# Kernel tuning notes

Hardware: AMD Instinct MI355X
Metric: run time of the kernel (lower is better)

## Reference

```python
import jax, jax.numpy as jnp
import numpy as np

D_MODEL = 1024
N_HEAD = 16
HEAD_SIZE = D_MODEL // N_HEAD
LAYER_ID = 12
N_LAYER = 24
HEAD_SIZE_DIVISOR = 8
TM_DIM = 32   # TIME_MIX_EXTRA_DIM
TD_DIM = 64   # TIME_DECAY_EXTRA_DIM
B, T = 4, 1024
EPS = 1e-5 * HEAD_SIZE_DIVISOR ** 2


def setup_inputs() -> dict:
    key = jax.random.key(0)
    ks = jax.random.split(key, 12)
    C = D_MODEL
    r0 = LAYER_ID / (N_LAYER - 1)
    r1 = 1.0 - LAYER_ID / N_LAYER
    ddd = np.arange(C, dtype=np.float64) / C
    time_maa_x = (1.0 - ddd ** r1).astype(np.float32)
    time_maa_w = (1.0 - ddd ** r1).astype(np.float32)
    time_maa_k = (1.0 - ddd ** r1).astype(np.float32)
    time_maa_v = (1.0 - (ddd ** r1 + 0.3 * r0)).astype(np.float32)
    time_maa_r = (1.0 - ddd ** (0.5 * r1)).astype(np.float32)
    time_maa_g = (1.0 - ddd ** (0.5 * r1)).astype(np.float32)
    n = np.arange(C, dtype=np.float64)
    time_decay = (-6.0 + 5.0 * (n / (C - 1)) ** (0.7 + 1.3 * r0)).astype(np.float32)
    zig = ((n + 1) % 3 - 1) * 0.1
    time_faaaa = (r0 * (1 - n / (C - 1)) + zig).astype(np.float32).reshape(N_HEAD, HEAD_SIZE)
    s = 1.0 / np.sqrt(C)
    inp = {
        "x": jax.random.normal(ks[0], (B, T, C), jnp.float32),
        "time_maa_x": jnp.asarray(time_maa_x),
        "time_maa_w": jnp.asarray(time_maa_w),
        "time_maa_k": jnp.asarray(time_maa_k),
        "time_maa_v": jnp.asarray(time_maa_v),
        "time_maa_r": jnp.asarray(time_maa_r),
        "time_maa_g": jnp.asarray(time_maa_g),
        "time_maa_w1": jax.random.uniform(ks[1], (C, TM_DIM * 5), jnp.float32, -0.01, 0.01),
        "time_maa_w2": jax.random.uniform(ks[2], (5, TM_DIM, C), jnp.float32, -0.01, 0.01),
        "time_decay": jnp.asarray(time_decay),
        "time_decay_w1": jax.random.uniform(ks[3], (C, TD_DIM), jnp.float32, -0.01, 0.01),
        "time_decay_w2": jax.random.uniform(ks[4], (TD_DIM, C), jnp.float32, -0.01, 0.01),
        "time_faaaa": jnp.asarray(time_faaaa),
        "W_r": jax.random.normal(ks[5], (C, C), jnp.float32) * s,
        "W_k": jax.random.normal(ks[6], (C, C), jnp.float32) * s,
        "W_v": jax.random.normal(ks[7], (C, C), jnp.float32) * s,
        "W_g": jax.random.normal(ks[8], (C, C), jnp.float32) * s,
        "W_o": jax.random.normal(ks[9], (C, C), jnp.float32) * s,
        "ln_gamma": jnp.ones((C,), jnp.float32),
        "ln_beta": jnp.zeros((C,), jnp.float32),
    }
    return inp


def _wkv6(r, k, v, w, u):
    # r,k,v,w: (B,T,H,K); u: (H,K). Sequential data-dependent linear attention.
    Bc, Tc, H, K = r.shape
    wdec = jnp.exp(-jnp.exp(w))  # decay in (0,1)

    def step(S, inp):
        r_t, k_t, v_t, wd_t = inp           # each (B,H,K)
        kv = k_t[:, :, :, None] * v_t[:, :, None, :]   # (B,H,K,K) key x value
        y = jnp.einsum('bhk,bhkj->bhj', r_t, S + u[None, :, :, None] * kv)
        S = S * wd_t[:, :, :, None] + kv    # decay along key dim, then accumulate
        return S, y

    S0 = jnp.zeros((Bc, H, K, K), r.dtype)
    xs = (jnp.swapaxes(r, 0, 1), jnp.swapaxes(k, 0, 1),
          jnp.swapaxes(v, 0, 1), jnp.swapaxes(wdec, 0, 1))
    _, ys = jax.lax.scan(step, S0, xs)      # ys: (T,B,H,K)
    return jnp.swapaxes(ys, 0, 1).reshape(Bc, Tc, H * K)


def reference(x, time_maa_x, time_maa_w, time_maa_k, time_maa_v, time_maa_r,
              time_maa_g, time_maa_w1, time_maa_w2, time_decay, time_decay_w1,
              time_decay_w2, time_faaaa, W_r, W_k, W_v, W_g, W_o, ln_gamma, ln_beta):
    Bc, Tc, C = x.shape
    H, K = N_HEAD, HEAD_SIZE
    # token shift: state[t] = x[t-1], zero at t=0
    xs = jnp.pad(x, ((0, 0), (1, 0), (0, 0)))[:, :-1]
    xx = xs - x
    # LoRA-style data-dependent mixing coefficients
    xxx = x + xx * time_maa_x
    m = jnp.tanh(xxx @ time_maa_w1).reshape(Bc, Tc, 5, TM_DIM)
    m = jnp.einsum('btfe,fec->fbtc', m, time_maa_w2)  # (5,B,T,C)
    mw, mk, mv, mr, mg = m[0], m[1], m[2], m[3], m[4]
    xw = x + xx * (time_maa_w + mw)
    xk = x + xx * (time_maa_k + mk)
    xv = x + xx * (time_maa_v + mv)
    xr = x + xx * (time_maa_r + mr)
    xg = x + xx * (time_maa_g + mg)
    r = xr @ W_r
    k = xk @ W_k
    v = xv @ W_v
    g = jax.nn.silu(xg @ W_g)
    w = time_decay + jnp.tanh(xw @ time_decay_w1) @ time_decay_w2
    y = _wkv6(r.reshape(Bc, Tc, H, K), k.reshape(Bc, Tc, H, K),
              v.reshape(Bc, Tc, H, K), w.reshape(Bc, Tc, H, K), time_faaaa)
    # GroupNorm with H groups over channel dim (per (b,t) position)
    yg = y.reshape(Bc, Tc, H, K)
    mu = jnp.mean(yg, axis=-1, keepdims=True)
    var = jnp.mean((yg - mu) ** 2, axis=-1, keepdims=True)
    yn = ((yg - mu) / jnp.sqrt(var + EPS)).reshape(Bc, Tc, C)
    yn = yn * ln_gamma + ln_beta
    return (yn * g) @ W_o
```

## Files before the change

kernel.cpp:

```cpp
#include <hip/hip_runtime.h>

#define Bb 4
#define Tt 1024
#define Cc 1024
#define Hh 16
#define BT (Bb*Tt)
#define CHUNK 32
#define NCH (Tt/CHUNK)

typedef unsigned int uint;
typedef unsigned short u16;
typedef __bf16 bf16x8 __attribute__((ext_vector_type(8)));
typedef float f32x4 __attribute__((ext_vector_type(4)));
typedef const __attribute__((address_space(1))) uint GU;
typedef __attribute__((address_space(3))) uint LU;

__device__ __forceinline__ float blo(uint u) { return __uint_as_float(u << 16); }
__device__ __forceinline__ float bhi(uint u) { return __uint_as_float(u & 0xffff0000u); }
__device__ __forceinline__ float b2f(u16 u) { return __uint_as_float(((uint)u) << 16); }
__device__ __forceinline__ u16 f2b(float f) {
  uint u = __float_as_uint(f);
  return (u16)((u + 0x7fffu + ((u >> 16) & 1u)) >> 16);
}
__device__ __forceinline__ float fast_tanh(float x) {
  float e = __expf(2.f * x);
  return 1.f - 2.f / (e + 1.f);
}

struct WPair { const float* s; u16* d; int K; int N; };
struct WPack { WPair p[9]; };

__global__ __launch_bounds__(256) void prep_transW(WPack wp,
    const float* __restrict__ x, const float* __restrict__ maa_x,
    u16* __restrict__ xxx)
{
  __shared__ float tile[32][33];
  if (blockIdx.z < 9) {
    WPair pr = wp.p[blockIdx.z];
    int c0 = blockIdx.x*32, r0 = blockIdx.y*32;
    if (c0 >= pr.N || r0 >= pr.K) return;
    int tc = threadIdx.x & 31, tr = threadIdx.x >> 5;
    #pragma unroll
    for (int p = 0; p < 4; ++p)
      tile[tr + p*8][tc] = pr.s[(size_t)(r0 + tr + p*8)*pr.N + c0 + tc];
    __syncthreads();
    #pragma unroll
    for (int p = 0; p < 4; ++p) {
      int n = tr + p*8;
      pr.d[(size_t)(c0 + n)*pr.K + r0 + tc] = f2b(tile[tc][n]);
    }
  } else {
    int vb = (blockIdx.z - 9)*1024 + blockIdx.y*32 + blockIdx.x;
    int idx = vb*256 + threadIdx.x;
    int c4 = idx & 255;
    int bt = idx >> 8;
    int t = bt & (Tt-1);
    float4 xc = ((const float4*)x)[idx];
    float4 xp = make_float4(0.f,0.f,0.f,0.f);
    if (t > 0) xp = ((const float4*)x)[idx - 256];
    float4 mx = ((const float4*)maa_x)[c4];
    ushort4 o;
    o.x = f2b(fmaf(xp.x - xc.x, mx.x, xc.x));
    o.y = f2b(fmaf(xp.y - xc.y, mx.y, xc.y));
    o.z = f2b(fmaf(xp.z - xc.z, mx.z, xc.z));
    o.w = f2b(fmaf(xp.w - xc.w, mx.w, xc.w));
    ((ushort4*)xxx)[idx] = o;
  }
}

__global__ __launch_bounds__(256) void mix_mfma(
    const float* __restrict__ x, const float* __restrict__ m1p,
    const u16* __restrict__ w2T,
    const float* __restrict__ maa_w, const float* __restrict__ maa_k,
    const float* __restrict__ maa_v, const float* __restrict__ maa_r,
    const float* __restrict__ maa_g,
    u16* __restrict__ xw, u16* __restrict__ xk, u16* __restrict__ xv,
    u16* __restrict__ xr, u16* __restrict__ xg)
{
  __shared__ __align__(16) u16 strip[4][16][72];
  const int tid = threadIdx.x;
  const int lane = tid & 63;
  const int wv = tid >> 6;
  const int sid = blockIdx.x*4 + wv;
  const int rs = sid >> 4, cs = sid & 15;
  const int r0 = rs*16, c0 = cs*64;
  const int fr = lane & 15, kc = lane >> 4;

  float xc[4][4], xd[4][4];
  #pragma unroll
  for (int n = 0; n < 4; ++n) {
    int col = c0 + n*16 + fr;
    #pragma unroll
    for (int q = 0; q < 4; ++q) {
      int row = r0 + kc*4 + q;
      size_t o = (size_t)row*Cc + col;
      float v = x[o];
      float p = ((row & (Tt-1)) != 0) ? x[o - Cc] : 0.f;
      xc[n][q] = v;
      xd[n][q] = p - v;
    }
  }

  const size_t aBase = (size_t)(r0 + fr)*160 + kc*8;
  u16* const outs[5] = {xw, xk, xv, xr, xg};
  const float* const maas[5] = {maa_w, maa_k, maa_v, maa_r, maa_g};

  #pragma unroll
  for (int f = 0; f < 5; ++f) {
    float s8[8] = {0.f,0.f,0.f,0.f,0.f,0.f,0.f,0.f};
    #pragma unroll
    for (int z = 0; z < 4; ++z) {
      const float4* p = (const float4*)(m1p + (size_t)z*655360 + aBase + f*32);
      float4 a = p[0], b = p[1];
      s8[0]+=a.x; s8[1]+=a.y; s8[2]+=a.z; s8[3]+=a.w;
      s8[4]+=b.x; s8[5]+=b.y; s8[6]+=b.z; s8[7]+=b.w;
    }
    u16 t8[8];
    #pragma unroll
    for (int j = 0; j < 8; ++j) t8[j] = f2b(fast_tanh(s8[j]));
    bf16x8 af = *(const bf16x8*)t8;
    f32x4 acc[4];
    #pragma unroll
    for (int n = 0; n < 4; ++n) {
      bf16x8 bg = *(const bf16x8*)(w2T + (size_t)(c0 + n*16 + fr)*160 + f*32 + kc*8);
      acc[n] = __builtin_amdgcn_mfma_f32_16x16x32_bf16(af, bg, f32x4{0.f,0.f,0.f,0.f}, 0, 0, 0);
    }
    const float* __restrict__ ma = maas[f];
    u16* __restrict__ op = outs[f];
    #pragma unroll
    for (int n = 0; n < 4; ++n) {
      int colL = n*16 + fr;
      float mv = ma[c0 + colL];
      #pragma unroll
      for (int q = 0; q < 4; ++q)
        strip[wv][kc*4 + q][colL] = f2b(fmaf(xd[n][q], mv + acc[n][q], xc[n][q]));
    }
    #pragma unroll
    for (int rd = 0; rd < 2; ++rd) {
      int r8 = (lane >> 3) + rd*8;
      uint4 v = *(const uint4*)&strip[wv][r8][(lane & 7)*8];
      *(uint4*)(op + (size_t)(r0 + r8)*Cc + c0 + (lane & 7)*8) = v;
    }
  }
}

template<bool OUTF32>
__device__ __forceinline__ void mfma_core(
    const u16* __restrict__ A, const u16* __restrict__ Bt,
    void* __restrict__ Cout, const float* __restrict__ bias,
    int ld, int kloop, int N, int act)
{
  __shared__ __align__(16) u16 lds[2][2][128*32];
  const int tid = threadIdx.x;
  const int lane = tid & 63;
  const int wv = __builtin_amdgcn_readfirstlane(tid >> 6);

  const int nby8 = gridDim.y >> 3;
  const int i_lin = blockIdx.y * gridDim.x + blockIdx.x;
  const int cx = i_lin & 7, rest = i_lin >> 3;
  const int bm = (cx * nby8 + rest % nby8) * 128;
  const int bn = (rest / nby8) * 128;

  const int wm = (wv >> 1) * 64;
  const int wn = (wv & 1) * 64;
  const int kc = lane >> 4;
  const int fr = lane & 15;

  const int srow = wv*16 + (lane >> 2);
  const int ssw  = (srow >> 1) & 3;
  const int scol = ((lane & 3) ^ ssw) * 8;
  const size_t aoff = (size_t)(bm + srow) * ld + scol;
  const size_t boff = (size_t)(bn + srow) * ld + scol;

#define STAGE(bufi, kt) do { \
    size_t ko_ = (size_t)(kt) * 32; \
    __builtin_amdgcn_global_load_lds((GU*)(A + aoff + ko_), \
        (LU*)&lds[bufi][0][wv*512], 16, 0, 0); \
    __builtin_amdgcn_global_load_lds((GU*)(A + aoff + (size_t)64*ld + ko_), \
        (LU*)&lds[bufi][0][wv*512 + 64*32], 16, 0, 0); \
    __builtin_amdgcn_global_load_lds((GU*)(Bt + boff + ko_), \
        (LU*)&lds[bufi][1][wv*512], 16, 0, 0); \
    __builtin_amdgcn_global_load_lds((GU*)(Bt + boff + (size_t)64*ld + ko_), \
        (LU*)&lds[bufi][1][wv*512 + 64*32], 16, 0, 0); \
  } while(0)

  int ard[4], brd[4];
  #pragma unroll
  for (int m = 0; m < 4; ++m) {
    int ra = wm + m*16 + fr;
    int rb = wn + m*16 + fr;
    ard[m] = ra*32 + (kc ^ ((ra >> 1) & 3))*8;
    brd[m] = rb*32 + (kc ^ ((rb >> 1) & 3))*8;
  }

  f32x4 acc[4][4];
  #pragma unroll
  for (int m = 0; m < 4; ++m)
    #pragma unroll
    for (int n = 0; n < 4; ++n)
      acc[m][n] = f32x4{0.f, 0.f, 0.f, 0.f};

  const int NK = kloop >> 5;
  STAGE(0, 0);
  __syncthreads();
  int buf = 0;
  for (int kt = 0; kt < NK; ++kt) {
    if (kt + 1 < NK) STAGE(buf^1, kt+1);
    bf16x8 af[4], bg[4];
    #pragma unroll
    for (int m = 0; m < 4; ++m) af[m] = *(const bf16x8*)&lds[buf][0][ard[m]];
    #pragma unroll
    for (int n = 0; n < 4; ++n) bg[n] = *(const bf16x8*)&lds[buf][1][brd[n]];
    #pragma unroll
    for (int m = 0; m < 4; ++m)
      #pragma unroll
      for (int n = 0; n < 4; ++n)
        acc[m][n] = __builtin_amdgcn_mfma_f32_16x16x32_bf16(af[m], bg[n], acc[m][n], 0, 0, 0);
    __syncthreads();
    buf ^= 1;
  }
#undef STAGE

  const int orow = bm + wm + (lane >> 4) * 4;
  const int ocol = bn + wn + fr;
  #pragma unroll
  for (int m = 0; m < 4; ++m) {
    #pragma unroll
    for (int n = 0; n < 4; ++n) {
      int col = ocol + n*16;
      if (col < N) {
        float bs = bias ? bias[col] : 0.f;
        #pragma unroll
        for (int q = 0; q < 4; ++q) {
          float vv = acc[m][n][q] + bs;
          if (act == 1) vv = tanhf(vv);
          else if (act == 2) vv = vv / (1.f + __expf(-vv));
          size_t off = (size_t)(orow + m*16 + q) * N + col;
          if (OUTF32) ((float*)Cout)[off] = vv;
          else ((u16*)Cout)[off] = f2b(vv);
        }
      }
    }
  }
}

template<int ACT, bool OUTF32>
__global__ __launch_bounds__(256) void gemm_mfma(
    const u16* __restrict__ A, const u16* __restrict__ Bt,
    void* __restrict__ Cout, const float* __restrict__ bias, int K, int N)
{
  mfma_core<OUTF32>(A, Bt, Cout, bias, K, K, N, ACT);
}

__global__ __launch_bounds__(256) void gemm_ksplit(
    const u16* __restrict__ A, const u16* __restrict__ Bt,
    float* __restrict__ Cp, int ld, int ksz, int N)
{
  const int z = blockIdx.z;
  mfma_core<true>(A + (size_t)z*ksz, Bt + (size_t)z*ksz,
                  Cp + (size_t)z*4096*N, nullptr, ld, ksz, N, 0);
}

struct GPack { const u16* A[4]; const u16* B[4]; u16* C[4]; };

#define VMW(n) asm volatile("s_waitcnt vmcnt(" #n ")" ::: "memory")
#define LGKM0() asm volatile("s_waitcnt lgkmcnt(0)" ::: "memory")
#define SCHB() __builtin_amdgcn_sched_barrier(0)
#define HBAR() __builtin_amdgcn_s_barrier()

__global__ __launch_bounds__(512) void gemm_rkvg256(GPack gp) {
  __shared__ __align__(16) u16 lds[2][2][2][8192];
  const int z = blockIdx.z;
  const u16* __restrict__ Ap  = gp.A[z];
  const u16* __restrict__ Btp = gp.B[z];
  u16* __restrict__ Cp = gp.C[z];
  const int act = (z == 3) ? 2 : 0;

  const int tid = threadIdx.x;
  const int lane = tid & 63;
  const int wv = __builtin_amdgcn_readfirstlane(tid >> 6);

  const int i_lin = blockIdx.y * gridDim.x + blockIdx.x;
  const int tile = (i_lin & 7) * 8 + (i_lin >> 3);
  const int bm = (tile >> 2) * 256;
  const int bn = (tile & 3) * 256;

  const int wm = (wv >> 2) * 128;
  const int wn = (wv & 3) * 64;
  const int kc = lane >> 4;
  const int fr = lane & 15;

  const int srow0 = (wv*2 + 0)*16 + (lane >> 2);
  const int srow1 = (wv*2 + 1)*16 + (lane >> 2);
  const int sc0 = ((lane & 3) ^ ((srow0 >> 1) & 3)) * 8;
  const int sc1 = ((lane & 3) ^ ((srow1 >> 1) & 3)) * 8;
  const size_t aoff0 = (size_t)(bm + srow0)*Cc + sc0;
  const size_t aoff1 = (size_t)(bm + srow1)*Cc + sc1;
  const size_t boff0 = (size_t)(bn + srow0)*Cc + sc0;
  const size_t boff1 = (size_t)(bn + srow1)*Cc + sc1;

  int ard[8], brd[4];
  #pragma unroll
  for (int mh = 0; mh < 2; ++mh)
    #pragma unroll
    for (int mf = 0; mf < 4; ++mf) {
      int r = wm + mh*64 + mf*16 + fr;
      ard[mh*4+mf] = r*32 + (kc ^ ((r >> 1) & 3))*8;
    }
  #pragma unroll
  for (int nf = 0; nf < 4; ++nf) {
    int r = wn + nf*16 + fr;
    brd[nf] = r*32 + (kc ^ ((r >> 1) & 3))*8;
  }

  f32x4 acc[8][4];
  #pragma unroll
  for (int m = 0; m < 8; ++m)
    #pragma unroll
    for (int n = 0; n < 4; ++n)
      acc[m][n] = f32x4{0.f, 0.f, 0.f, 0.f};

#define STG256(DB, MAT, KH, kt, off0, off1, src) do { \
    u16* dst_ = &lds[(DB)][(MAT)][(KH)][wv*1024]; \
    __builtin_amdgcn_global_load_lds((GU*)((src) + (off0) + (size_t)(kt)*64 + (KH)*32), \
        (LU*)dst_, 16, 0, 0); \
    __builtin_amdgcn_global_load_lds((GU*)((src) + (off1) + (size_t)(kt)*64 + (KH)*32), \
        (LU*)(dst_ + 512), 16, 0, 0); \
  } while(0)

#define PH256(cur, KH, MH, LOADB, STMAT, STKH, DOSTAGE, VMTOK) do { \
    _Pragma("unroll") \
    for (int mf = 0; mf < 4; ++mf) \
      af[mf] = *(const bf16x8*)&lds[(cur)][0][KH][ard[(MH)*4+mf]]; \
    if (LOADB) { \
      _Pragma("unroll") \
      for (int nf = 0; nf < 4; ++nf) \
        bg[nf] = *(const bf16x8*)&lds[(cur)][1][KH][brd[nf]]; \
    } \
    if (DOSTAGE) { \
      if ((STMAT) == 0) STG256((cur)^1, 0, STKH, t+1, aoff0, aoff1, Ap); \
      else              STG256((cur)^1, 1, STKH, t+1, boff0, boff1, Btp); \
    } \
    VMTOK; \
    SCHB(); \
    HBAR(); \
    LGKM0(); \
    SCHB(); \
    __builtin_amdgcn_s_setprio(1); \
    _Pragma("unroll") \
    for (int mf = 0; mf < 4; ++mf) \
      _Pragma("unroll") \
      for (int nf = 0; nf < 4; ++nf) \
        acc[(MH)*4+mf][nf] = __builtin_amdgcn_mfma_f32_16x16x32_bf16(af[mf], bg[nf], acc[(MH)*4+mf][nf], 0, 0, 0); \
    __builtin_amdgcn_s_setprio(0); \
    SCHB(); \
    HBAR(); \
  } while(0)

  const int NK = Cc >> 6;

  STG256(0, 0, 0, 0, aoff0, aoff1, Ap);
  STG256(0, 1, 0, 0, boff0, boff1, Btp);
  STG256(0, 0, 1, 0, aoff0, aoff1, Ap);
  STG256(0, 1, 1, 0, boff0, boff1, Btp);
  VMW(4);
  SCHB();
  HBAR();

  bf16x8 af[4], bg[4];
  int t;
  #pragma unroll 2
  for (t = 0; t < NK - 1; ++t) {
    const int cur = t & 1;
    PH256(cur, 0, 0, true,  0, 0, true,  (void)0);
    PH256(cur, 0, 1, false, 1, 0, true,  VMW(4));
    PH256(cur, 1, 0, true,  0, 1, true,  (void)0);
    PH256(cur, 1, 1, false, 1, 1, true,  VMW(4));
  }
  {
    const int cur = t & 1;
    PH256(cur, 0, 0, true,  0, 0, false, (void)0);
    PH256(cur, 0, 1, false, 0, 0, false, VMW(0));
    PH256(cur, 1, 0, true,  0, 0, false, (void)0);
    PH256(cur, 1, 1, false, 0, 0, false, (void)0);
  }
#undef PH256
#undef STG256

  const int orow = bm + wm + (lane >> 4) * 4;
  const int ocol = bn + wn + fr;
  #pragma unroll
  for (int m = 0; m < 8; ++m) {
    #pragma unroll
    for (int nf = 0; nf < 4; ++nf) {
      #pragma unroll
      for (int q = 0; q < 4; ++q) {
        float vv = acc[m][nf][q];
        if (act == 2) vv = vv / (1.f + __expf(-vv));
        Cp[(size_t)(orow + (m >> 2)*64 + (m & 3)*16 + q) * Cc + ocol + nf*16] = f2b(vv);
      }
    }
  }
}

__global__ __launch_bounds__(256) void wkv_pass1(u16* __restrict__ r,
    const u16* __restrict__ k, const u16* __restrict__ v,
    const float* __restrict__ wl1p, const u16* __restrict__ tdw2T,
    const float* __restrict__ tdecay, const float* __restrict__ u,
    u16* __restrict__ y, u16* __restrict__ S, float* __restrict__ D)
{
  __shared__ __align__(16) u16 rS[CHUNK][72];
  __shared__ __align__(16) u16 kS[CHUNK][72];
  __shared__ __align__(16) u16 vS[CHUNK][72];
  __shared__ __align__(16) u16 aW[CHUNK][72];
  __shared__ __align__(16) float bufEW[CHUNK][68];
  __shared__ __align__(16) float eKnL[CHUNK][68];
  __shared__ __align__(16) u16 Rt[CHUNK][72];
  __shared__ __align__(16) u16 Kt[CHUNK][72];
  __shared__ __align__(16) u16 Ru[CHUNK][72];
  __shared__ __align__(16) u16 KhT[64][40];
  __shared__ __align__(16) u16 VT[64][40];
  __shared__ __align__(16) u16 A_lds[CHUNK][40];
  __shared__ float uL[64];
  __shared__ float Dl[64];

  const int blk = blockIdx.x;
  const int chunk = blk & (NCH-1);
  const int bh = blk >> 5;
  const int h = bh & (Hh-1);
  const int b = bh >> 4;
  const int tid = threadIdx.x;
  const int lane = tid & 63;
  const int wv = tid >> 6;
  const int fr = lane & 15;
  const int kc = lane >> 4;

  const int trow0 = b*Tt + chunk*CHUNK;
  const size_t rowbase = (size_t)trow0*Cc + h*64;
  {
    int tt = tid >> 3, c8 = (tid & 7)*8;
    size_t go = rowbase + (size_t)tt*Cc + c8;
    *(uint4*)&rS[tt][c8] = *(const uint4*)(r + go);
    *(uint4*)&kS[tt][c8] = *(const uint4*)(k + go);
    *(uint4*)&vS[tt][c8] = *(const uint4*)(v + go);
    size_t wrow = (size_t)(trow0 + tt)*64 + c8;
    float s8[8] = {0.f,0.f,0.f,0.f,0.f,0.f,0.f,0.f};
    #pragma unroll
    for (int z = 0; z < 4; ++z) {
      const float4* p = (const float4*)(wl1p + (size_t)z*262144 + wrow);
      float4 a = p[0], b2 = p[1];
      s8[0]+=a.x; s8[1]+=a.y; s8[2]+=a.z; s8[3]+=a.w;
      s8[4]+=b2.x; s8[5]+=b2.y; s8[6]+=b2.z; s8[7]+=b2.w;
    }
    u16 t8[8];
    #pragma unroll
    for (int j = 0; j < 8; ++j) t8[j] = f2b(fast_tanh(s8[j]));
    *(uint4*)&aW[tt][c8] = *(const uint4*)t8;
  }
  if (tid < 64) uL[tid] = u[h*64 + tid];
  __syncthreads();

  {
    const int icol = wv*16 + fr;
    const float bs = tdecay[h*64 + icol];
    #pragma unroll
    for (int tb = 0; tb < 2; ++tb) {
      f32x4 acc = {0.f,0.f,0.f,0.f};
      #pragma unroll
      for (int ks = 0; ks < 2; ++ks) {
        bf16x8 a  = *(const bf16x8*)&aW[tb*16+fr][kc*8 + ks*32];
        bf16x8 bb = *(const bf16x8*)(tdw2T + (size_t)(h*64 + icol)*64 + ks*32 + kc*8);
        acc = __builtin_amdgcn_mfma_f32_16x16x32_bf16(a, bb, acc, 0, 0, 0);
      }
      #pragma unroll
      for (int q = 0; q < 4; ++q)
        bufEW[tb*16 + kc*4 + q][icol] = __expf(acc[q] + bs);
    }
  }
  __syncthreads();

  if (tid < 64) {
    float eR = 1.f;
    for (int t = 0; t < CHUNK; ++t) {
      float e = bufEW[t][tid];
      bufEW[t][tid] = eR;
      eR *= __expf(-e);
      eKnL[t][tid] = __builtin_amdgcn_rcpf(eR);
    }
    Dl[tid] = eR;
    D[(size_t)blk*64 + tid] = eR;
  }
  __syncthreads();

  {
    int t = tid >> 3, i0 = (tid & 7)*8;
    uint4 rv4 = *(const uint4*)&rS[t][i0];
    uint4 kv4 = *(const uint4*)&kS[t][i0];
    const uint* rw = (const uint*)&rv4;
    const uint* kw = (const uint*)&kv4;
    u16 rt8[8], kt8[8], ru8[8];
    #pragma unroll
    for (int q = 0; q < 8; ++q) {
      int i = i0 + q;
      float rv = (q & 1) ? bhi(rw[q>>1]) : blo(rw[q>>1]);
      float kv = (q & 1) ? bhi(kw[q>>1]) : blo(kw[q>>1]);
      float eR = bufEW[t][i];
      float eKn = eKnL[t][i];
      float ktv = kv * eKn;
      rt8[q] = f2b(rv * eR);
      kt8[q] = f2b(ktv);
      ru8[q] = f2b(rv * uL[i]);
      KhT[i][t] = f2b(ktv * Dl[i]);
      VT[i][t] = vS[t][i];
    }
    *(uint4*)&Rt[t][i0] = *(const uint4*)rt8;
    *(uint4*)&Kt[t][i0] = *(const uint4*)kt8;
    *(uint4*)&Ru[t][i0] = *(const uint4*)ru8;
  }
  __syncthreads();

  {
    const int wr = wv >> 1, wc = wv & 1;
    f32x4 accA = {0.f,0.f,0.f,0.f};
    f32x4 accD = {0.f,0.f,0.f,0.f};
    #pragma unroll
    for (int ks = 0; ks < 2; ++ks) {
      bf16x8 a  = *(const bf16x8*)&Rt[wr*16+fr][kc*8 + ks*32];
      bf16x8 bb = *(const bf16x8*)&Kt[wc*16+fr][kc*8 + ks*32];
      accA = __builtin_amdgcn_mfma_f32_16x16x32_bf16(a, bb, accA, 0, 0, 0);
      bf16x8 a2 = *(const bf16x8*)&Ru[wr*16+fr][kc*8 + ks*32];
      bf16x8 b2 = *(const bf16x8*)&kS[wc*16+fr][kc*8 + ks*32];
      accD = __builtin_amdgcn_mfma_f32_16x16x32_bf16(a2, b2, accD, 0, 0, 0);
    }
    #pragma unroll
    for (int q = 0; q < 4; ++q) {
      int trow = wr*16 + kc*4 + q;
      int scol = wc*16 + fr;
      float val = (scol < trow) ? accA[q] : ((scol == trow) ? accD[q] : 0.f);
      A_lds[trow][scol] = f2b(val);
    }
  }
  __syncthreads();

  #pragma unroll
  for (int tb = 0; tb < 2; ++tb) {
    bf16x8 a  = *(const bf16x8*)&A_lds[tb*16+fr][kc*8];
    bf16x8 bb = *(const bf16x8*)&VT[wv*16+fr][kc*8];
    f32x4 acc = {0.f,0.f,0.f,0.f};
    acc = __builtin_amdgcn_mfma_f32_16x16x32_bf16(a, bb, acc, 0, 0, 0);
    #pragma unroll
    for (int q = 0; q < 4; ++q) {
      int t = tb*16 + kc*4 + q;
      int j = wv*16 + fr;
      y[rowbase + (size_t)t*Cc + j] = f2b(acc[q]);
    }
  }
  #pragma unroll
  for (int jb = 0; jb < 4; ++jb) {
    bf16x8 a  = *(const bf16x8*)&KhT[wv*16+fr][kc*8];
    bf16x8 bb = *(const bf16x8*)&VT[jb*16+fr][kc*8];
    f32x4 acc = {0.f,0.f,0.f,0.f};
    acc = __builtin_amdgcn_mfma_f32_16x16x32_bf16(a, bb, acc, 0, 0, 0);
    #pragma unroll
    for (int q = 0; q < 4; ++q) {
      int i = wv*16 + kc*4 + q;
      int j = jb*16 + fr;
      S[((size_t)blk*64 + i)*64 + j] = f2b(acc[q]);
    }
  }
  {
    int tt = tid >> 3, c8 = (tid & 7)*8;
    *(uint4*)(r + rowbase + (size_t)tt*Cc + c8) = *(const uint4*)&Rt[tt][c8];
  }
}

__global__ __launch_bounds__(256) void wkv_pass2(u16* __restrict__ S,
    const float* __restrict__ D)
{
  __shared__ float Dl[NCH][64];
  const int bh = blockIdx.x >> 2;
  const int jq = blockIdx.x & 3;
  const int tid = threadIdx.x;
  {
    const float4* src = (const float4*)(D + (size_t)bh*NCH*64);
    float4* dst = (float4*)&Dl[0][0];
    dst[tid] = src[tid];
    dst[tid + 256] = src[tid + 256];
  }
  __syncthreads();
  const int j = jq*16 + (tid & 15);
  const int i0 = (tid >> 4) * 4;
  const size_t base0 = (((size_t)bh*NCH)*64 + i0)*64 + j;
  u16 tmp[NCH][4];
  #pragma unroll
  for (int c = 0; c < NCH; ++c) {
    size_t base = base0 + (size_t)c*4096;
    #pragma unroll
    for (int ii = 0; ii < 4; ++ii) tmp[c][ii] = S[base + ii*64];
  }
  float Sr[4] = {0.f, 0.f, 0.f, 0.f};
  #pragma unroll
  for (int c = 0; c < NCH; ++c) {
    size_t base = base0 + (size_t)c*4096;
    #pragma unroll
    for (int ii = 0; ii < 4; ++ii) {
      S[base + ii*64] = f2b(Sr[ii]);
      Sr[ii] = fmaf(Sr[ii], Dl[c][i0+ii], b2f(tmp[c][ii]));
    }
  }
}

__global__ __launch_bounds__(256) void gn_gate(const u16* __restrict__ y,
   const u16* __restrict__ g, const u16* __restrict__ rc, const u16* __restrict__ S,
   const float* __restrict__ gamma, const float* __restrict__ beta, u16* __restrict__ out)
{
  __shared__ u16 rcl[8][Cc];
  const int bt0 = blockIdx.x * 8;
  const int b = bt0 >> 10;
  const int t0 = bt0 & (Tt-1);
  const int chunk = t0 >> 5;
  const int tid = threadIdx.x;
  #pragma unroll
  for (int rr = 0; rr < 8; ++rr)
    ((ushort4*)rcl[rr])[tid] = ((const ushort4*)(rc + (size_t)(bt0+rr)*Cc))[tid];
  __syncthreads();
  const int c0 = tid*4, h = c0 >> 6, j0 = c0 & 63;
  const u16* Sb = S + (((size_t)(b*Hh + h)*NCH + chunk)*64)*64 + j0;
  float corr[8][4];
  #pragma unroll
  for (int rr = 0; rr < 8; ++rr)
    #pragma unroll
    for (int q = 0; q < 4; ++q) corr[rr][q] = 0.f;
  #pragma unroll 4
  for (int i = 0; i < 64; ++i) {
    ushort4 sv = *(const ushort4*)(Sb + (size_t)i*64);
    float s0 = b2f(sv.x), s1 = b2f(sv.y), s2 = b2f(sv.z), s3 = b2f(sv.w);
    #pragma unroll
    for (int rr = 0; rr < 8; ++rr) {
      float rv = b2f(rcl[rr][h*64 + i]);
      corr[rr][0] = fmaf(rv, s0, corr[rr][0]);
      corr[rr][1] = fmaf(rv, s1, corr[rr][1]);
      corr[rr][2] = fmaf(rv, s2, corr[rr][2]);
      corr[rr][3] = fmaf(rv, s3, corr[rr][3]);
    }
  }
  float4 ga = ((const float4*)gamma)[tid];
  float4 be = ((const float4*)beta)[tid];
  #pragma unroll
  for (int rr = 0; rr < 8; ++rr) {
    size_t o4 = (size_t)(bt0+rr)*(Cc/4) + tid;
    ushort4 yv4 = ((const ushort4*)y)[o4];
    float y0 = b2f(yv4.x) + corr[rr][0];
    float y1 = b2f(yv4.y) + corr[rr][1];
    float y2 = b2f(yv4.z) + corr[rr][2];
    float y3 = b2f(yv4.w) + corr[rr][3];
    float s  = y0 + y1 + y2 + y3;
    float sq = y0*y0 + y1*y1 + y2*y2 + y3*y3;
    #pragma unroll
    for (int m = 1; m < 16; m <<= 1) {
      s  += __shfl_xor(s, m, 64);
      sq += __shfl_xor(sq, m, 64);
    }
    float mu  = s * (1.f/64.f);
    float var = sq * (1.f/64.f) - mu*mu;
    float rstd = rsqrtf(var + 6.4e-4f);
    ushort4 gu = ((const ushort4*)g)[o4];
    ushort4 ou;
    ou.x = f2b(((y0 - mu)*rstd*ga.x + be.x) * b2f(gu.x));
    ou.y = f2b(((y1 - mu)*rstd*ga.y + be.y) * b2f(gu.y));
    ou.z = f2b(((y2 - mu)*rstd*ga.z + be.z) * b2f(gu.z));
    ou.w = f2b(((y3 - mu)*rstd*ga.w + be.w) * b2f(gu.w));
    ((ushort4*)out)[o4] = ou;
  }
}

extern "C" void kernel_launch(void* const* d_in, const int* in_sizes, int n_in,
                              void* d_out, int out_size, void* d_ws, size_t ws_size,
                              hipStream_t stream) {
  const float* x      = (const float*)d_in[0];
  const float* maa_x  = (const float*)d_in[1];
  const float* maa_w  = (const float*)d_in[2];
  const float* maa_k  = (const float*)d_in[3];
  const float* maa_v  = (const float*)d_in[4];
  const float* maa_r  = (const float*)d_in[5];
  const float* maa_g  = (const float*)d_in[6];
  const float* w1     = (const float*)d_in[7];
  const float* w2     = (const float*)d_in[8];
  const float* tdecay = (const float*)d_in[9];
  const float* tdw1   = (const float*)d_in[10];
  const float* tdw2   = (const float*)d_in[11];
  const float* faaaa  = (const float*)d_in[12];
  const float* Wr     = (const float*)d_in[13];
  const float* Wk     = (const float*)d_in[14];
  const float* Wv     = (const float*)d_in[15];
  const float* Wg     = (const float*)d_in[16];
  const float* Wo     = (const float*)d_in[17];
  const float* gamma  = (const float*)d_in[18];
  const float* beta   = (const float*)d_in[19];
  float* out = (float*)d_out;

  const size_t MB = 1u << 20;
  char* wsb = (char*)d_ws;
  float* m1p  = (float*)(wsb + 0);
  float* wl1p = (float*)(wsb + 0);
  u16*   w2T  = (u16*)(wsb + 12*MB);
  u16*   xk   = (u16*)(wsb + 16*MB);
  u16*   xv   = (u16*)(wsb + 24*MB);
  u16*   xr   = (u16*)(wsb + 32*MB);
  u16*   xg   = (u16*)(wsb + 40*MB);
  u16*   xw   = (u16*)(wsb + 48*MB);
  u16*   rbuf = (u16*)(wsb + 56*MB);
  u16*   kbuf = (u16*)(wsb + 64*MB);
  u16*   vbuf = (u16*)(wsb + 72*MB);
  u16*   gbuf = (u16*)(wsb + 80*MB);
  float* Dbuf = (float*)(wsb + 88*MB);
  u16*   Sbuf = (u16*)(wsb + 16*MB);
  u16*   BW0  = (u16*)(wsb + 88*MB + 512*1024);
  u16*   BW1  = (u16*)((char*)BW0 + 2*MB);
  u16*   BW2  = (u16*)((char*)BW1 + 2*MB);
  u16*   BW3  = (u16*)((char*)BW2 + 2*MB);
  u16*   BW4  = (u16*)((char*)BW3 + 2*MB);
  u16*   w1T  = (u16*)((char*)BW4 + 2*MB);
  u16*   tdw1T = (u16*)(wsb + 99*MB);
  u16*   tdw2T = (u16*)(wsb + 99*MB + 256*1024);
  u16*   gated = xr;
  u16*   xxx16 = (u16*)d_out;
  u16*   yb16  = (u16*)d_out;

  dim3 blk(256);
  WPack wp;
  wp.p[0] = {Wr, BW0, Cc, Cc};  wp.p[1] = {Wk, BW1, Cc, Cc};
  wp.p[2] = {Wv, BW2, Cc, Cc};  wp.p[3] = {Wg, BW3, Cc, Cc};
  wp.p[4] = {Wo, BW4, Cc, Cc};  wp.p[5] = {w1, w1T, Cc, 160};
  wp.p[6] = {tdw1, tdw1T, Cc, 64}; wp.p[7] = {tdw2, tdw2T, 64, Cc};
  wp.p[8] = {w2, w2T, 160, Cc};
  prep_transW<<<dim3(32,32,13), blk, 0, stream>>>(wp, x, maa_x, xxx16);
  gemm_ksplit<<<dim3(2, 32, 4), blk, 0, stream>>>(xxx16, w1T, m1p, Cc, 256, 160);
  mix_mfma<<<1024, blk, 0, stream>>>(x, m1p, w2T, maa_w, maa_k, maa_v, maa_r, maa_g,
                                     xw, xk, xv, xr, xg);
  gemm_ksplit<<<dim3(1, 32, 4), blk, 0, stream>>>(xw, tdw1T, wl1p, Cc, 256, 64);
  GPack gp;
  gp.A[0] = xr; gp.A[1] = xk; gp.A[2] = xv; gp.A[3] = xg;
  gp.B[0] = BW0; gp.B[1] = BW1; gp.B[2] = BW2; gp.B[3] = BW3;
  gp.C[0] = rbuf; gp.C[1] = kbuf; gp.C[2] = vbuf; gp.C[3] = gbuf;
  gemm_rkvg256<<<dim3(4, 16, 4), dim3(512), 0, stream>>>(gp);
  wkv_pass1<<<Bb*Hh*NCH, blk, 0, stream>>>(rbuf, kbuf, vbuf, wl1p, tdw2T, tdecay,
                                           faaaa, yb16, Sbuf, Dbuf);
  wkv_pass2<<<Bb*Hh*4, blk, 0, stream>>>(Sbuf, Dbuf);
  gn_gate<<<BT/8, blk, 0, stream>>>(yb16, gbuf, rbuf, Sbuf, gamma, beta, gated);
  gemm_mfma<0,true><<<dim3(8, 32), blk, 0, stream>>>(gated, BW4, out, nullptr, Cc, Cc);
}
```

Baseline: 188.9 us.

## Stage LoRA tanh and shifted x tiles in LDS; coalesce WKV chunk stores

The mix kernel now has each block cover a 16x256 tile. It cooperatively sums the split-K m1 partials, applies tanh once into shared memory, and loads the shifted x rows into an LDS tile. Previously each wave recomputed the partial sums and tanh, and read x and x[t-1] separately from global memory. The WKV chunk kernel now writes its y and S outputs through LDS (reusing the kS/rS/vS buffers) so the global stores are 16-byte coalesced instead of scattered 2-byte writes. This adds LDS usage and extra barriers, which may reduce occupancy.

```diff
diff --git a/kernel.cpp b/kernel.cpp
--- a/kernel.cpp
+++ b/kernel.cpp
@@ -77,48 +77,66 @@
     u16* __restrict__ xw, u16* __restrict__ xk, u16* __restrict__ xv,
     u16* __restrict__ xr, u16* __restrict__ xg)
 {
+  __shared__ __align__(16) u16 aW[16][168];
+  __shared__ __align__(16) float xS[17][260];
   __shared__ __align__(16) u16 strip[4][16][72];
   const int tid = threadIdx.x;
   const int lane = tid & 63;
   const int wv = tid >> 6;
-  const int sid = blockIdx.x*4 + wv;
-  const int rs = sid >> 4, cs = sid & 15;
-  const int r0 = rs*16, c0 = cs*64;
+  const int rs = blockIdx.x >> 2;
+  const int cb = blockIdx.x & 3;
+  const int r0 = rs*16;
+  const int c0b = cb*256;
   const int fr = lane & 15, kc = lane >> 4;
-
+  const bool firstrow = (r0 & (Tt-1)) == 0;
+
+  for (int task = tid; task < 640; task += 256) {
+    int f  = task >> 7;
+    int r  = (task >> 3) & 15;
+    int c4 = task & 7;
+    size_t off = (size_t)(r0 + r)*160 + f*32 + c4*4;
+    float4 s = *(const float4*)(m1p + off);
+    #pragma unroll
+    for (int z = 1; z < 4; ++z) {
+      float4 p = *(const float4*)(m1p + (size_t)z*655360 + off);
+      s.x += p.x; s.y += p.y; s.z += p.z; s.w += p.w;
+    }
+    ushort4 t4;
+    t4.x = f2b(fast_tanh(s.x)); t4.y = f2b(fast_tanh(s.y));
+    t4.z = f2b(fast_tanh(s.z)); t4.w = f2b(fast_tanh(s.w));
+    *(ushort4*)&aW[r][f*32 + c4*4] = t4;
+  }
+  for (int i = tid; i < 1088; i += 256) {
+    int r17 = i >> 6;
+    int c4  = i & 63;
+    float4 v = make_float4(0.f,0.f,0.f,0.f);
+    if (!(r17 == 0 && firstrow))
+      v = *(const float4*)(x + (size_t)(r0 - 1 + r17)*Cc + c0b + c4*4);
+    *(float4*)&xS[r17][c4*4] = v;
+  }
+  __syncthreads();
+
+  const int c0 = c0b + wv*64;
   float xc[4][4], xd[4][4];
   #pragma unroll
   for (int n = 0; n < 4; ++n) {
-    int col = c0 + n*16 + fr;
+    int cl = wv*64 + n*16 + fr;
     #pragma unroll
     for (int q = 0; q < 4; ++q) {
-      int row = r0 + kc*4 + q;
-      size_t o = (size_t)row*Cc + col;
-      float v = x[o];
-      float p = ((row & (Tt-1)) != 0) ? x[o - Cc] : 0.f;
+      int rl = kc*4 + q;
+      float v = xS[rl + 1][cl];
+      float p = xS[rl][cl];
       xc[n][q] = v;
       xd[n][q] = p - v;
     }
   }
 
-  const size_t aBase = (size_t)(r0 + fr)*160 + kc*8;
   u16* const outs[5] = {xw, xk, xv, xr, xg};
   const float* const maas[5] = {maa_w, maa_k, maa_v, maa_r, maa_g};
 
   #pragma unroll
   for (int f = 0; f < 5; ++f) {
-    float s8[8] = {0.f,0.f,0.f,0.f,0.f,0.f,0.f,0.f};
-    #pragma unroll
-    for (int z = 0; z < 4; ++z) {
-      const float4* p = (const float4*)(m1p + (size_t)z*655360 + aBase + f*32);
-      float4 a = p[0], b = p[1];
-      s8[0]+=a.x; s8[1]+=a.y; s8[2]+=a.z; s8[3]+=a.w;
-      s8[4]+=b.x; s8[5]+=b.y; s8[6]+=b.z; s8[7]+=b.w;
-    }
-    u16 t8[8];
-    #pragma unroll
-    for (int j = 0; j < 8; ++j) t8[j] = f2b(fast_tanh(s8[j]));
-    bf16x8 af = *(const bf16x8*)t8;
+    bf16x8 af = *(const bf16x8*)&aW[fr][f*32 + kc*8];
     f32x4 acc[4];
     #pragma unroll
     for (int n = 0; n < 4; ++n) {
@@ -549,11 +567,8 @@
     f32x4 acc = {0.f,0.f,0.f,0.f};
     acc = __builtin_amdgcn_mfma_f32_16x16x32_bf16(a, bb, acc, 0, 0, 0);
     #pragma unroll
-    for (int q = 0; q < 4; ++q) {
-      int t = tb*16 + kc*4 + q;
-      int j = wv*16 + fr;
-      y[rowbase + (size_t)t*Cc + j] = f2b(acc[q]);
-    }
+    for (int q = 0; q < 4; ++q)
+      kS[tb*16 + kc*4 + q][wv*16 + fr] = f2b(acc[q]);
   }
   #pragma unroll
   for (int jb = 0; jb < 4; ++jb) {
@@ -563,10 +578,22 @@
     acc = __builtin_amdgcn_mfma_f32_16x16x32_bf16(a, bb, acc, 0, 0, 0);
     #pragma unroll
     for (int q = 0; q < 4; ++q) {
-      int i = wv*16 + kc*4 + q;
+      int i = kc*4 + q;
       int j = jb*16 + fr;
-      S[((size_t)blk*64 + i)*64 + j] = f2b(acc[q]);
-    }
+      if (wv < 2) rS[wv*16 + i][j] = f2b(acc[q]);
+      else        vS[(wv-2)*16 + i][j] = f2b(acc[q]);
+    }
+  }
+  __syncthreads();
+  {
+    int row = tid >> 3, seg = tid & 7;
+    *(uint4*)(y + rowbase + (size_t)row*Cc + seg*8) = *(const uint4*)&kS[row][seg*8];
+  }
+  #pragma unroll
+  for (int rd = 0; rd < 2; ++rd) {
+    int row = tid >> 2, s8 = (tid & 3) + rd*4;
+    const u16* src = (row < 32) ? &rS[row][s8*8] : &vS[row-32][s8*8];
+    *(uint4*)(S + ((size_t)blk*64 + row)*64 + s8*8) = *(const uint4*)src;
   }
   {
     int tt = tid >> 3, c8 = (tid & 7)*8;
```

New measurement: 180.2 us. 1.05x faster.
